# Optimization experiments

Hardware: AMD Instinct MI355X
Metric: run time of the kernel (lower is better)

Reference implementation:

```python
import jax, jax.numpy as jnp
import numpy as np

N_NODES = 20000
N_EDGES = 640000
D = 128          # vision_dim == topo_dim
OUT = 256        # out_dim
B = 64           # image batch == num graphs
HW = 64
NEG_SLOPE = 0.2


def _sn(w2d, u):
    """PyTorch spectral_norm forward: one power iteration (u,v detached), W/sigma."""
    v = jax.lax.stop_gradient(w2d.T @ u)
    v = v / (jnp.linalg.norm(v) + 1e-12)
    u2 = jax.lax.stop_gradient(w2d @ v)
    u2 = u2 / (jnp.linalg.norm(u2) + 1e-12)
    sigma = u2 @ (w2d @ v)
    return w2d / sigma


def _leaky(x):
    return jnp.where(x >= 0, x, NEG_SLOPE * x)


def setup_inputs() -> dict:
    key = jax.random.key(0)
    ks = jax.random.split(key, 16)
    vis = jax.random.normal(ks[0], (B, D, HW, HW), dtype=jnp.float32)
    topo = jax.random.normal(ks[1], (N_NODES, D), dtype=jnp.float32)
    edge_index = jax.random.randint(ks[2], (2, N_EDGES), 0, N_NODES, dtype=jnp.int64)
    batch = jnp.sort(jax.random.randint(ks[3], (N_NODES,), 0, B, dtype=jnp.int64))
    s = 0.05
    conv_w = jax.random.normal(ks[4], (D, D, 3, 3), dtype=jnp.float32) * s
    conv_b = jnp.zeros((D,), dtype=jnp.float32)
    conv_u = jax.random.normal(ks[5], (D,), dtype=jnp.float32)
    fcv_w = jax.random.normal(ks[6], (OUT, D * 4), dtype=jnp.float32) * s
    fcv_b = jnp.zeros((OUT,), dtype=jnp.float32)
    fcv_u = jax.random.normal(ks[7], (OUT,), dtype=jnp.float32)
    gcn_w = jax.random.normal(ks[8], (D, D), dtype=jnp.float32) * s
    gcn_b = jnp.zeros((D,), dtype=jnp.float32)
    fct_w = jax.random.normal(ks[9], (OUT, D), dtype=jnp.float32) * s
    fct_b = jnp.zeros((OUT,), dtype=jnp.float32)
    fct_u = jax.random.normal(ks[10], (OUT,), dtype=jnp.float32)
    return dict(vis=vis, topo=topo, edge_index=edge_index, batch=batch,
                conv_w=conv_w, conv_b=conv_b, conv_u=conv_u,
                fcv_w=fcv_w, fcv_b=fcv_b, fcv_u=fcv_u,
                gcn_w=gcn_w, gcn_b=gcn_b,
                fct_w=fct_w, fct_b=fct_b, fct_u=fct_u)


def reference(vis, topo, edge_index, batch,
              conv_w, conv_b, conv_u,
              fcv_w, fcv_b, fcv_u,
              gcn_w, gcn_b,
              fct_w, fct_b, fct_u):
    # ---- vision head: spectral-norm conv3x3 -> leaky_relu -> adaptive max pool 2x2 -> SN linear
    cw = _sn(conv_w.reshape(D, -1), conv_u).reshape(conv_w.shape)
    x = jax.lax.conv_general_dilated(vis, cw, window_strides=(1, 1), padding='VALID',
                                     dimension_numbers=('NCHW', 'OIHW', 'NCHW'))
    x = _leaky(x + conv_b[None, :, None, None])              # [B, D, 62, 62]
    Bc, C, H, W = x.shape
    x = x.reshape(Bc, C, 2, H // 2, 2, W // 2).max(axis=(3, 5))  # adaptive max pool -> [B,D,2,2]
    x = x.reshape(Bc, -1)                                    # [B, 4D]
    vis_score = x @ _sn(fcv_w, fcv_u).T + fcv_b              # [B, OUT]

    # ---- topo head: GCNConv (sym-norm, self-loops) -> leaky_relu -> global max pool -> SN linear
    n = topo.shape[0]
    loop = jnp.arange(n, dtype=edge_index.dtype)
    src = jnp.concatenate([edge_index[0], loop])
    dst = jnp.concatenate([edge_index[1], loop])
    deg = jax.ops.segment_sum(jnp.ones_like(dst, dtype=topo.dtype), dst, num_segments=n)
    dis = jnp.where(deg > 0, jax.lax.rsqrt(jnp.maximum(deg, 1.0)), 0.0)
    norm = dis[src] * dis[dst]                               # [E+N]
    xw = topo @ gcn_w                                        # [N, D]
    h = jax.ops.segment_sum(norm[:, None] * xw[src], dst, num_segments=n) + gcn_b
    h = _leaky(h)
    pooled = jax.ops.segment_max(h, batch, num_segments=B)   # [B, D]
    topo_score = pooled @ _sn(fct_w, fct_u).T + fct_b        # [B, OUT]

    return (vis_score, topo_score)
```

## Files before the change

### kernel.cpp

```cpp
#include <hip/hip_runtime.h>
#include <hip/hip_bf16.h>
#include <float.h>
#include <stdint.h>

#define NB   64
#define CD   128
#define OUTD 256
#define NNODE 20000
#define NEDGE 640000

typedef __bf16 bf16x8 __attribute__((ext_vector_type(8)));
typedef __bf16 bf16x4 __attribute__((ext_vector_type(4)));
typedef float  f32x4  __attribute__((ext_vector_type(4)));

__device__ inline void gl_lds16(const void* g, void* l) {
  __builtin_amdgcn_global_load_lds(
      (const __attribute__((address_space(1))) void*)g,
      (__attribute__((address_space(3))) void*)l, 16, 0, 0);
}

__device__ inline void atomicMaxF(float* addr, float val) {
  if (val >= 0.f) atomicMax((int*)addr, __float_as_int(val));
  else            atomicMin((unsigned int*)addr, __float_as_uint(val));
}

__global__ void k_init(float* __restrict__ pooled_v, float* __restrict__ pooled_t,
                       int* __restrict__ cnt, int* __restrict__ fill,
                       float* __restrict__ sn_scratch, int* __restrict__ ntotal) {
  const int i = blockIdx.x * 256 + threadIdx.x;
  if (i < NB * CD * 4) pooled_v[i] = -FLT_MAX;
  if (i < NB * CD)     pooled_t[i] = -FLT_MAX;
  if (i < NNODE)       { cnt[i] = 0; fill[i] = 0; }
  if (i < 1796)        sn_scratch[i] = 0.0f;
  if (i == 0)          *ntotal = 0;
}

__global__ __launch_bounds__(256) void k_sn_v(const float* __restrict__ conv_w, const float* __restrict__ conv_u,
                                              const float* __restrict__ fcv_w,  const float* __restrict__ fcv_u,
                                              const float* __restrict__ fct_w,  const float* __restrict__ fct_u,
                                              float* __restrict__ sn) {
  const int bb = blockIdx.x;
  const float* W; const float* u; float* v; int C; int r0;
  if (bb < 16)      { W = conv_w; u = conv_u; v = sn;        C = 1152; r0 = bb * 8; }
  else if (bb < 48) { W = fcv_w;  u = fcv_u;  v = sn + 1152; C = 512;  r0 = (bb - 16) * 8; }
  else              { W = fct_w;  u = fct_u;  v = sn + 1664; C = 128;  r0 = (bb - 48) * 8; }
  const int tid = threadIdx.x;
  float acc[5] = {0.f, 0.f, 0.f, 0.f, 0.f};
  for (int i = r0; i < r0 + 8; ++i) {
    const float ui = u[i];
    const float* row = W + (size_t)i * C;
    #pragma unroll
    for (int t = 0; t < 5; ++t) {
      const int j = tid + t * 256;
      if (j < C) acc[t] += ui * row[j];
    }
  }
  #pragma unroll
  for (int t = 0; t < 5; ++t) {
    const int j = tid + t * 256;
    if (j < C) atomicAdd(&v[j], acc[t]);
  }
}

__global__ __launch_bounds__(256) void k_sn_w(const float* __restrict__ conv_w,
                                              const float* __restrict__ fcv_w,
                                              const float* __restrict__ fct_w,
                                              float* __restrict__ sn) {
  const int gw = blockIdx.x * 4 + (threadIdx.x >> 6);
  const int lane = threadIdx.x & 63;
  const float* W; const float* v; int C, m, row;
  if (gw < 128)      { W = conv_w; v = sn;        C = 1152; m = 0; row = gw; }
  else if (gw < 384) { W = fcv_w;  v = sn + 1152; C = 512;  m = 1; row = gw - 128; }
  else               { W = fct_w;  v = sn + 1664; C = 128;  m = 2; row = gw - 384; }
  const float* wr = W + (size_t)row * C;
  float y = 0.f;
  for (int c = lane; c < C; c += 64) y += wr[c] * v[c];
  #pragma unroll
  for (int s = 32; s > 0; s >>= 1) y += __shfl_xor(y, s, 64);
  if (lane == 0) atomicAdd(&sn[1792 + m], y * y);
}

__global__ __launch_bounds__(256) void k_sn_fin(const float* __restrict__ sn, float* __restrict__ inv_sigma) {
  __shared__ float red[256];
  const int tid = threadIdx.x;
  const int off[4] = {0, 1152, 1664, 1792};
  for (int m = 0; m < 3; ++m) {
    const int C = off[m + 1] - off[m];
    float ss = 0.f;
    for (int j = tid; j < C; j += 256) { const float a = sn[off[m] + j]; ss += a * a; }
    red[tid] = ss; __syncthreads();
    for (int s = 128; s > 0; s >>= 1) { if (tid < s) red[tid] += red[tid + s]; __syncthreads(); }
    if (tid == 0) inv_sigma[m] = (sqrtf(red[0]) + 1e-12f) / sqrtf(sn[1792 + m]);
    __syncthreads();
  }
}

__global__ __launch_bounds__(256, 2) void k_prep(const float* __restrict__ vis, __bf16* __restrict__ visT2,
                                                 const float* __restrict__ conv_w, const float* __restrict__ inv_sigma,
                                                 __hip_bfloat16* __restrict__ Bt2,
                                                 const int* __restrict__ dst, int* __restrict__ cnt) {
  __shared__ __bf16 tile[32768];
  const int bid = blockIdx.x;
  const int t = threadIdx.x;
  if (bid < 1024) {
    const int b = bid >> 4, y0 = (bid & 15) << 2;
    const int wave = t >> 6, lane = t & 63;
    const float* src = vis + (size_t)b * 524288 + y0 * 64 + lane * 4;
    #pragma unroll
    for (int i = 0; i < 32; ++i) {
      const int c = wave * 32 + i;
      const f32x4 v = *(const f32x4*)(src + (size_t)c * 4096);
      bf16x4 o;
      #pragma unroll
      for (int k = 0; k < 4; ++k) o[k] = (__bf16)v[k];
      *(bf16x4*)&tile[c * 256 + lane * 4] = o;
    }
    __syncthreads();
    #pragma unroll
    for (int yy = 0; yy < 4; ++yy) {
      bf16x8* dstv = (bf16x8*)(visT2 + ((size_t)((b << 6) + y0 + yy) << 13));
      #pragma unroll
      for (int k = 0; k < 4; ++k) {
        const int j = k * 256 + t;
        const int g = j >> 6, x = j & 63;
        union { bf16x8 v; __bf16 h[8]; } u;
        #pragma unroll
        for (int cc = 0; cc < 8; ++cc)
          u.h[cc] = tile[(g * 8 + cc) * 256 + yy * 64 + x];
        dstv[j] = u.v;
      }
    }
  } else if (bid < 1600) {
    const int tt = (bid - 1024) * 256 + t;
    if (tt < 147456) {
      const int j = tt & 7, n = (tt >> 3) & 127, s = (tt >> 10) & 7, hk = (tt >> 13) & 1, tap = tt >> 14;
      const int ci = hk * 64 + s * 8 + j;
      Bt2[tt] = __float2bfloat16(conv_w[n * 1152 + ci * 9 + tap] * inv_sigma[0]);
    }
  } else {
    const int e = (bid - 1600) * 256 + t;
    if (e < NEDGE) atomicAdd(&cnt[dst[e]], 1);
  }
}

__global__ __launch_bounds__(256, 4) void k_convb(const __hip_bfloat16* __restrict__ visT2,
                                                  const __hip_bfloat16* __restrict__ Bt2,
                                                  const float* __restrict__ conv_b,
                                                  float* __restrict__ pooled_v,
                                                  const int* __restrict__ srcE, const int* __restrict__ dstE,
                                                  const int* __restrict__ offset, int* __restrict__ fill,
                                                  int* __restrict__ sorted_src) {
  __shared__ bf16x8 lds_a[1024];
  __shared__ bf16x8 lds_b[1024];
  const int bid = blockIdx.x;
  if (bid >= 1984) {
    const int e = (bid - 1984) * 256 + threadIdx.x;
    if (e < NEDGE) {
      const int tt = dstE[e];
      const int pos = atomicAdd(&fill[tt], 1);
      sorted_src[offset[tt] + pos] = srcE[e];
    }
    return;
  }
  const int bx = bid;
  const int b = bx / 31;
  const int y0 = (bx % 31) * 2;
  const int tid = threadIdx.x;
  const int wave = tid >> 6, lane = tid & 63;
  const int quad = lane >> 4, l15 = lane & 15;

  f32x4 acc[8][2];
  #pragma unroll
  for (int i = 0; i < 8; ++i) {
    acc[i][0] = f32x4{0.f, 0.f, 0.f, 0.f};
    acc[i][1] = f32x4{0.f, 0.f, 0.f, 0.f};
  }

  const __hip_bfloat16* vb = visT2 + ((size_t)b << 19);
  const int s0 = wave << 1;
  bf16x8* ldsA0 = &lds_a[s0 << 7];
  bf16x8* ldsB0 = &lds_b[s0 << 7];
  const int lane8 = lane << 3;

  for (int ky = 0; ky < 3; ++ky) {
    for (int kx = 0; kx < 3; ++kx) {
      const int tap = ky * 3 + kx;
      #pragma unroll
      for (int hk = 0; hk < 2; ++hk) {
        const __hip_bfloat16* a0p = vb + ((size_t)(((y0 + ky) << 4) + (hk << 3) + s0) << 9) + (kx << 3) + lane8;
        const __hip_bfloat16* a1p = vb + ((size_t)(((y0 + 1 + ky) << 4) + (hk << 3) + s0) << 9) + (kx << 3) + lane8;
        const __hip_bfloat16* bp  = Bt2 + (((size_t)(((tap << 1) + hk) << 3) + s0) << 10) + lane8;
        gl_lds16(a0p,        ldsA0);
        gl_lds16(a1p,        ldsA0 + 64);
        gl_lds16(a0p + 512,  ldsA0 + 128);
        gl_lds16(a1p + 512,  ldsA0 + 192);
        gl_lds16(bp,         ldsB0);
        gl_lds16(bp + 512,   ldsB0 + 64);
        gl_lds16(bp + 1024,  ldsB0 + 128);
        gl_lds16(bp + 1536,  ldsB0 + 192);
        __syncthreads();
        const bf16x8 b00 = lds_b[(quad << 7) + (wave << 5) + l15];
        const bf16x8 b01 = lds_b[(quad << 7) + (wave << 5) + 16 + l15];
        const bf16x8 b10 = lds_b[((4 + quad) << 7) + (wave << 5) + l15];
        const bf16x8 b11 = lds_b[((4 + quad) << 7) + (wave << 5) + 16 + l15];
        #pragma unroll
        for (int mt = 0; mt < 8; ++mt) {
          const bf16x8 a0 = lds_a[(quad << 7) + (mt << 4) + l15];
          const bf16x8 a1 = lds_a[((4 + quad) << 7) + (mt << 4) + l15];
          acc[mt][0] = __builtin_amdgcn_mfma_f32_16x16x32_bf16(a0, b00, acc[mt][0], 0, 0, 0);
          acc[mt][1] = __builtin_amdgcn_mfma_f32_16x16x32_bf16(a0, b01, acc[mt][1], 0, 0, 0);
          acc[mt][0] = __builtin_amdgcn_mfma_f32_16x16x32_bf16(a1, b10, acc[mt][0], 0, 0, 0);
          acc[mt][1] = __builtin_amdgcn_mfma_f32_16x16x32_bf16(a1, b11, acc[mt][1], 0, 0, 0);
        }
        __syncthreads();
      }
    }
  }

  const float cb0 = conv_b[(wave << 5) + l15];
  const float cb1 = conv_b[(wave << 5) + 16 + l15];
  float pmax[2][2][2];
  #pragma unroll
  for (int i = 0; i < 8; ++i) (&pmax[0][0][0])[i] = -FLT_MAX;

  #pragma unroll
  for (int mt = 0; mt < 8; ++mt) {
    const int py = (y0 + (mt >> 2)) >= 31 ? 1 : 0;
    #pragma unroll
    for (int r = 0; r < 4; ++r) {
      const int x = ((mt & 3) << 4) + (quad << 2) + r;
      if (x < 62) {
        const int px = x >= 31 ? 1 : 0;
        float v0 = acc[mt][0][r] + cb0;  v0 = v0 >= 0.f ? v0 : 0.2f * v0;
        float v1 = acc[mt][1][r] + cb1;  v1 = v1 >= 0.f ? v1 : 0.2f * v1;
        pmax[0][py][px] = fmaxf(pmax[0][py][px], v0);
        pmax[1][py][px] = fmaxf(pmax[1][py][px], v1);
      }
    }
  }
  #pragma unroll
  for (int nt = 0; nt < 2; ++nt)
    #pragma unroll
    for (int py = 0; py < 2; ++py)
      #pragma unroll
      for (int px = 0; px < 2; ++px) {
        float v = pmax[nt][py][px];
        v = fmaxf(v, __shfl_xor(v, 16, 64));
        v = fmaxf(v, __shfl_xor(v, 32, 64));
        if (quad == 0) {
          const int n = (wave << 5) + (nt << 4) + l15;
          atomicMaxF(&pooled_v[(size_t)b * 512 + n * 4 + py * 2 + px], v);
        }
      }
}

__global__ __launch_bounds__(256) void k_scan_xw(const int* __restrict__ cnt, int* __restrict__ offset,
                                                 int* __restrict__ total, float* __restrict__ dis,
                                                 const float* __restrict__ topo, const float* __restrict__ gcn_w,
                                                 __bf16* __restrict__ xws) {
  __shared__ f32x4 w4[4096];
  __shared__ int sbase;
  const int tid = threadIdx.x;
  if (blockIdx.x < 79) {
    int* red = (int*)w4;
    const int n = blockIdx.x * 256 + tid;
    const int v = (n < NNODE) ? cnt[n] : 0;
    red[tid] = v; __syncthreads();
    for (int d = 1; d < 256; d <<= 1) {
      const int t = (tid >= d) ? red[tid - d] : 0;
      __syncthreads();
      red[tid] += t;
      __syncthreads();
    }
    if (tid == 255) sbase = atomicAdd(total, red[255]);
    __syncthreads();
    if (n < NNODE) {
      offset[n] = sbase + red[tid] - v;
      dis[n] = rsqrtf((float)(v + 1));
    }
  } else {
    const f32x4* gw4 = (const f32x4*)gcn_w;
    for (int i = tid; i < 4096; i += 256) w4[i] = gw4[i];
    __syncthreads();
    const int n0 = (blockIdx.x - 79) * 64;
    const int jq = tid & 31, ns = tid >> 5;
    for (int pass = 0; pass < 8; ++pass) {
      const int n = n0 + pass * 8 + ns;
      if (n >= NNODE) break;
      const f32x4* tr4 = (const f32x4*)(topo + (size_t)n * 128);
      f32x4 a = {0.f, 0.f, 0.f, 0.f};
      for (int d4 = 0; d4 < 32; ++d4) {
        const f32x4 t = tr4[d4];
        const int base = (d4 << 7) + jq;
        #pragma unroll
        for (int m = 0; m < 4; ++m) {
          const f32x4 w = w4[base + m * 32];
          #pragma unroll
          for (int k = 0; k < 4; ++k) a[k] += t[m] * w[k];
        }
      }
      const float dn = rsqrtf((float)(cnt[n] + 1));
      bf16x4 o;
      #pragma unroll
      for (int k = 0; k < 4; ++k) o[k] = (__bf16)(a[k] * dn);
      ((bf16x4*)xws)[(size_t)n * 32 + jq] = o;
    }
  }
}

__global__ __launch_bounds__(256) void k_gather(const int* __restrict__ sorted_src,
                                                const int* __restrict__ offset, const int* __restrict__ cnt,
                                                const float* __restrict__ dis, const __bf16* __restrict__ xws,
                                                const float* __restrict__ gcn_b, const int* __restrict__ batch,
                                                float* __restrict__ pooled_t) {
  __shared__ float hred[4][128];
  __shared__ int hg[4];
  const int wave = threadIdx.x >> 6, lane = threadIdx.x & 63;
  const int n = blockIdx.x * 4 + wave;
  const int slot = lane >> 4, l16 = lane & 15;
  const int e0 = offset[n], ne = cnt[n];
  const bf16x8* x8 = (const bf16x8*)xws;
  float a[8];
  if (slot == 0) {
    const bf16x8 v = x8[(size_t)n * 16 + l16];
    #pragma unroll
    for (int k = 0; k < 8; ++k) a[k] = (float)v[k];
  } else {
    #pragma unroll
    for (int k = 0; k < 8; ++k) a[k] = 0.f;
  }
  for (int e = slot; e < ne; e += 4) {
    const int s = sorted_src[e0 + e];
    const bf16x8 v = x8[(size_t)s * 16 + l16];
    #pragma unroll
    for (int k = 0; k < 8; ++k) a[k] += (float)v[k];
  }
  #pragma unroll
  for (int k = 0; k < 8; ++k) {
    a[k] += __shfl_xor(a[k], 16, 64);
    a[k] += __shfl_xor(a[k], 32, 64);
  }
  if (lane == 0) hg[wave] = batch[n];
  if (slot == 0) {
    const float dn = dis[n];
    #pragma unroll
    for (int k = 0; k < 8; ++k) {
      float t = gcn_b[(l16 << 3) + k] + dn * a[k];
      hred[wave][(l16 << 3) + k] = t >= 0.f ? t : 0.2f * t;
    }
  }
  __syncthreads();
  const int tid = threadIdx.x;
  if (tid < 128) {
    const int g0 = hg[0], g1 = hg[1], g2 = hg[2], g3 = hg[3];
    if (g0 == g1 && g1 == g2 && g2 == g3) {
      const float m = fmaxf(fmaxf(hred[0][tid], hred[1][tid]), fmaxf(hred[2][tid], hred[3][tid]));
      atomicMaxF(&pooled_t[g0 * 128 + tid], m);
    } else {
      atomicMaxF(&pooled_t[g0 * 128 + tid], hred[0][tid]);
      atomicMaxF(&pooled_t[g1 * 128 + tid], hred[1][tid]);
      atomicMaxF(&pooled_t[g2 * 128 + tid], hred[2][tid]);
      atomicMaxF(&pooled_t[g3 * 128 + tid], hred[3][tid]);
    }
  }
}

__global__ __launch_bounds__(256) void k_fc(const float* __restrict__ pooled_v, const float* __restrict__ fcv_w,
                                            const float* __restrict__ fcv_b,
                                            const float* __restrict__ pooled_t, const float* __restrict__ fct_w,
                                            const float* __restrict__ fct_b,
                                            const float* __restrict__ inv_sigma, float* __restrict__ out) {
  const int tid = threadIdx.x;
  if (blockIdx.x < 64) {
    __shared__ f32x4 xr[128];
    const int b = blockIdx.x;
    if (tid < 128) xr[tid] = ((const f32x4*)pooled_v)[b * 128 + tid];
    __syncthreads();
    const f32x4* wr = (const f32x4*)(fcv_w + (size_t)tid * 512);
    f32x4 a4 = {0.f, 0.f, 0.f, 0.f};
    for (int f = 0; f < 128; ++f) {
      const f32x4 x = xr[f];
      const f32x4 w = wr[f];
      #pragma unroll
      for (int k = 0; k < 4; ++k) a4[k] += x[k] * w[k];
    }
    const float a = a4[0] + a4[1] + a4[2] + a4[3];
    out[b * 256 + tid] = a * inv_sigma[1] + fcv_b[tid];
  } else {
    __shared__ f32x4 xr2[32];
    const int b = blockIdx.x - 64;
    if (tid < 32) xr2[tid] = ((const f32x4*)pooled_t)[b * 32 + tid];
    __syncthreads();
    const f32x4* wr = (const f32x4*)(fct_w + (size_t)tid * 128);
    f32x4 a4 = {0.f, 0.f, 0.f, 0.f};
    for (int f = 0; f < 32; ++f) {
      const f32x4 x = xr2[f];
      const f32x4 w = wr[f];
      #pragma unroll
      for (int k = 0; k < 4; ++k) a4[k] += x[k] * w[k];
    }
    const float a = a4[0] + a4[1] + a4[2] + a4[3];
    out[NB * 256 + b * 256 + tid] = a * inv_sigma[2] + fct_b[tid];
  }
}

extern "C" void kernel_launch(void* const* d_in, const int* in_sizes, int n_in,
                              void* d_out, int out_size, void* d_ws, size_t ws_size,
                              hipStream_t stream) {
  const float* vis    = (const float*)d_in[0];
  const float* topo   = (const float*)d_in[1];
  const int*   eidx   = (const int*)d_in[2];
  const int*   batch  = (const int*)d_in[3];
  const float* conv_w = (const float*)d_in[4];
  const float* conv_b = (const float*)d_in[5];
  const float* conv_u = (const float*)d_in[6];
  const float* fcv_w  = (const float*)d_in[7];
  const float* fcv_b  = (const float*)d_in[8];
  const float* fcv_u  = (const float*)d_in[9];
  const float* gcn_w  = (const float*)d_in[10];
  const float* gcn_b  = (const float*)d_in[11];
  const float* fct_w  = (const float*)d_in[12];
  const float* fct_b  = (const float*)d_in[13];
  const float* fct_u  = (const float*)d_in[14];
  float* out = (float*)d_out;

  char* p = (char*)d_ws;
  float* inv_sigma  = (float*)p; p += 256;
  float* sn_scratch = (float*)p; p += 1796 * 4 + 240;
  float* pooled_v   = (float*)p; p += (size_t)NB * 512 * 4;
  float* pooled_t   = (float*)p; p += (size_t)NB * 128 * 4;
  int*   cnt        = (int*)p;   p += (size_t)NNODE * 4;
  int*   offset     = (int*)p;   p += (size_t)NNODE * 4;
  int*   fill       = (int*)p;   p += (size_t)NNODE * 4;
  float* dis        = (float*)p; p += (size_t)NNODE * 4;
  int*   ntotal     = (int*)p;   p += 256;
  int*   sorted_src = (int*)p;   p += (size_t)NEDGE * 4;
  __bf16* xws       = (__bf16*)p; p += (size_t)NNODE * 128 * 2 + 256;
  __hip_bfloat16* Bt2 = (__hip_bfloat16*)p; p += (size_t)147456 * 2;
  p = (char*)(((uintptr_t)p + 255) & ~(uintptr_t)255);
  __bf16* visT2 = (__bf16*)p;

  hipLaunchKernelGGL(k_init,    dim3(128),  dim3(256), 0, stream, pooled_v, pooled_t, cnt, fill, sn_scratch, ntotal);
  hipLaunchKernelGGL(k_sn_v,    dim3(80),   dim3(256), 0, stream, conv_w, conv_u, fcv_w, fcv_u, fct_w, fct_u, sn_scratch);
  hipLaunchKernelGGL(k_sn_w,    dim3(160),  dim3(256), 0, stream, conv_w, fcv_w, fct_w, sn_scratch);
  hipLaunchKernelGGL(k_sn_fin,  dim3(1),    dim3(256), 0, stream, sn_scratch, inv_sigma);
  hipLaunchKernelGGL(k_prep,    dim3(4100), dim3(256), 0, stream, vis, visT2, conv_w, inv_sigma, Bt2, eidx + NEDGE, cnt);
  hipLaunchKernelGGL(k_scan_xw, dim3(392),  dim3(256), 0, stream, cnt, offset, ntotal, dis, topo, gcn_w, xws);
  hipLaunchKernelGGL(k_convb,   dim3(4484), dim3(256), 0, stream, (const __hip_bfloat16*)visT2, Bt2, conv_b, pooled_v,
                     eidx, eidx + NEDGE, offset, fill, sorted_src);
  hipLaunchKernelGGL(k_gather,  dim3(5000), dim3(256), 0, stream, sorted_src, offset, cnt, dis, xws, gcn_b, batch, pooled_t);
  hipLaunchKernelGGL(k_fc,      dim3(128),  dim3(256), 0, stream, pooled_v, fcv_w, fcv_b, pooled_t, fct_w, fct_b, inv_sigma, out);
}
```

Measured before the change: 475.7 us.

## Halve prep LDS tile, split conv into two launches, separate edge bucketing

The vis transpose in k_prep now runs in two channel phases with a 32KB LDS tile instead of 64KB, so launch bounds rise to 4 blocks per CU. The fused conv+bucket kernel is split: the conv runs as two launches of 32 images each, and edge bucketing moves to its own k_bucket kernel. This lets prep run at higher occupancy and keeps the atomic scatter from sharing a grid with the MFMA conv, at the cost of extra launches and an added barrier in prep.

```diff
diff --git a/kernel.cpp b/kernel.cpp
--- a/kernel.cpp
+++ b/kernel.cpp
@@ -95,11 +95,11 @@
   }
 }
 
-__global__ __launch_bounds__(256, 2) void k_prep(const float* __restrict__ vis, __bf16* __restrict__ visT2,
+__global__ __launch_bounds__(256, 4) void k_prep(const float* __restrict__ vis, __bf16* __restrict__ visT2,
                                                  const float* __restrict__ conv_w, const float* __restrict__ inv_sigma,
                                                  __hip_bfloat16* __restrict__ Bt2,
                                                  const int* __restrict__ dst, int* __restrict__ cnt) {
-  __shared__ __bf16 tile[32768];
+  __shared__ __bf16 tile[16384];
   const int bid = blockIdx.x;
   const int t = threadIdx.x;
   if (bid < 1024) {
@@ -107,28 +107,33 @@
     const int wave = t >> 6, lane = t & 63;
     const float* src = vis + (size_t)b * 524288 + y0 * 64 + lane * 4;
     #pragma unroll
-    for (int i = 0; i < 32; ++i) {
-      const int c = wave * 32 + i;
-      const f32x4 v = *(const f32x4*)(src + (size_t)c * 4096);
-      bf16x4 o;
-      #pragma unroll
-      for (int k = 0; k < 4; ++k) o[k] = (__bf16)v[k];
-      *(bf16x4*)&tile[c * 256 + lane * 4] = o;
-    }
-    __syncthreads();
-    #pragma unroll
-    for (int yy = 0; yy < 4; ++yy) {
-      bf16x8* dstv = (bf16x8*)(visT2 + ((size_t)((b << 6) + y0 + yy) << 13));
-      #pragma unroll
-      for (int k = 0; k < 4; ++k) {
-        const int j = k * 256 + t;
-        const int g = j >> 6, x = j & 63;
-        union { bf16x8 v; __bf16 h[8]; } u;
+    for (int ph = 0; ph < 2; ++ph) {
+      #pragma unroll
+      for (int i = 0; i < 16; ++i) {
+        const int cl = wave * 16 + i;
+        const int c = (ph << 6) + cl;
+        const f32x4 v = *(const f32x4*)(src + (size_t)c * 4096);
+        bf16x4 o;
         #pragma unroll
-        for (int cc = 0; cc < 8; ++cc)
-          u.h[cc] = tile[(g * 8 + cc) * 256 + yy * 64 + x];
-        dstv[j] = u.v;
-      }
+        for (int k = 0; k < 4; ++k) o[k] = (__bf16)v[k];
+        *(bf16x4*)&tile[cl * 256 + lane * 4] = o;
+      }
+      __syncthreads();
+      #pragma unroll
+      for (int yy = 0; yy < 4; ++yy) {
+        bf16x8* dstv = (bf16x8*)(visT2 + ((size_t)((b << 6) + y0 + yy) << 13)) + (ph << 9);
+        #pragma unroll
+        for (int k = 0; k < 2; ++k) {
+          const int j = k * 256 + t;
+          const int gl = j >> 6, x = j & 63;
+          union { bf16x8 v; __bf16 h[8]; } u;
+          #pragma unroll
+          for (int cc = 0; cc < 8; ++cc)
+            u.h[cc] = tile[(gl * 8 + cc) * 256 + yy * 64 + x];
+          dstv[j] = u.v;
+        }
+      }
+      if (ph == 0) __syncthreads();
     }
   } else if (bid < 1600) {
     const int tt = (bid - 1024) * 256 + t;
@@ -143,27 +148,14 @@
   }
 }
 
-__global__ __launch_bounds__(256, 4) void k_convb(const __hip_bfloat16* __restrict__ visT2,
-                                                  const __hip_bfloat16* __restrict__ Bt2,
-                                                  const float* __restrict__ conv_b,
-                                                  float* __restrict__ pooled_v,
-                                                  const int* __restrict__ srcE, const int* __restrict__ dstE,
-                                                  const int* __restrict__ offset, int* __restrict__ fill,
-                                                  int* __restrict__ sorted_src) {
+__global__ __launch_bounds__(256, 4) void k_conv(const __hip_bfloat16* __restrict__ visT2,
+                                                 const __hip_bfloat16* __restrict__ Bt2,
+                                                 const float* __restrict__ conv_b,
+                                                 float* __restrict__ pooled_v, int b0) {
   __shared__ bf16x8 lds_a[1024];
   __shared__ bf16x8 lds_b[1024];
-  const int bid = blockIdx.x;
-  if (bid >= 1984) {
-    const int e = (bid - 1984) * 256 + threadIdx.x;
-    if (e < NEDGE) {
-      const int tt = dstE[e];
-      const int pos = atomicAdd(&fill[tt], 1);
-      sorted_src[offset[tt] + pos] = srcE[e];
-    }
-    return;
-  }
-  const int bx = bid;
-  const int b = bx / 31;
+  const int bx = blockIdx.x;
+  const int b = b0 + bx / 31;
   const int y0 = (bx % 31) * 2;
   const int tid = threadIdx.x;
   const int wave = tid >> 6, lane = tid & 63;
@@ -308,6 +300,16 @@
   }
 }
 
+__global__ void k_bucket(const int* __restrict__ src, const int* __restrict__ dst,
+                         const int* __restrict__ offset, int* __restrict__ fill,
+                         int* __restrict__ sorted_src) {
+  const int e = blockIdx.x * 256 + threadIdx.x;
+  if (e >= NEDGE) return;
+  const int t = dst[e];
+  const int pos = atomicAdd(&fill[t], 1);
+  sorted_src[offset[t] + pos] = src[e];
+}
+
 __global__ __launch_bounds__(256) void k_gather(const int* __restrict__ sorted_src,
                                                 const int* __restrict__ offset, const int* __restrict__ cnt,
                                                 const float* __restrict__ dis, const __bf16* __restrict__ xws,
@@ -446,8 +448,9 @@
   hipLaunchKernelGGL(k_sn_fin,  dim3(1),    dim3(256), 0, stream, sn_scratch, inv_sigma);
   hipLaunchKernelGGL(k_prep,    dim3(4100), dim3(256), 0, stream, vis, visT2, conv_w, inv_sigma, Bt2, eidx + NEDGE, cnt);
   hipLaunchKernelGGL(k_scan_xw, dim3(392),  dim3(256), 0, stream, cnt, offset, ntotal, dis, topo, gcn_w, xws);
-  hipLaunchKernelGGL(k_convb,   dim3(4484), dim3(256), 0, stream, (const __hip_bfloat16*)visT2, Bt2, conv_b, pooled_v,
-                     eidx, eidx + NEDGE, offset, fill, sorted_src);
+  hipLaunchKernelGGL(k_conv,    dim3(32*31), dim3(256), 0, stream, (const __hip_bfloat16*)visT2, Bt2, conv_b, pooled_v, 0);
+  hipLaunchKernelGGL(k_conv,    dim3(32*31), dim3(256), 0, stream, (const __hip_bfloat16*)visT2, Bt2, conv_b, pooled_v, 32);
+  hipLaunchKernelGGL(k_bucket,  dim3(2500), dim3(256), 0, stream, eidx, eidx + NEDGE, offset, fill, sorted_src);
   hipLaunchKernelGGL(k_gather,  dim3(5000), dim3(256), 0, stream, sorted_src, offset, cnt, dis, xws, gcn_b, batch, pooled_t);
   hipLaunchKernelGGL(k_fc,      dim3(128),  dim3(256), 0, stream, pooled_v, fcv_w, fcv_b, pooled_t, fct_w, fct_b, inv_sigma, out);
 }
```

Measured after the change: 485.1 us. Within noise of the previous version (+2.0%).
